# Kernel optimization log

Measured on AMD Instinct MI355X. Metric: run time of the kernel, lower is better.

## Reference

```python
import jax, jax.numpy as jnp
import numpy as np

IN_CH, HID, OUT = 128, 128, 47

def _sage_conv(x_src, x_dst, src, dst, n_dst, Wl, bl, Wr):
    # mean aggregation of source features onto destination nodes
    msg_sum = jax.ops.segment_sum(x_src[src], dst, num_segments=n_dst)
    deg = jax.ops.segment_sum(jnp.ones((src.shape[0],), x_src.dtype), dst, num_segments=n_dst)
    agg = msg_sum / jnp.maximum(deg, 1.0)[:, None]
    return agg @ Wl + bl + x_dst @ Wr


def setup_inputs() -> dict:
    key = jax.random.key(0)
    ks = jax.random.split(key, 12)
    N0, N1, N2 = 200000, 100000, 20000
    E0, E1 = 1600000, 320000
    def glorot(k, fan_in, fan_out):
        s = jnp.sqrt(6.0 / (fan_in + fan_out))
        return jax.random.uniform(k, (fan_in, fan_out), jnp.float32, -s, s)
    return {
        'x': jax.random.normal(ks[0], (N0, IN_CH), jnp.float32),
        'src0': jax.random.randint(ks[1], (E0,), 0, N0),
        'dst0': jax.random.randint(ks[2], (E0,), 0, N1),
        'src1': jax.random.randint(ks[3], (E1,), 0, N1),
        'dst1': jax.random.randint(ks[4], (E1,), 0, N2),
        'n1': N1,
        'n2': N2,
        'Wl0': glorot(ks[5], IN_CH, HID),
        'bl0': jnp.zeros((HID,), jnp.float32),
        'Wr0': glorot(ks[6], IN_CH, HID),
        'Wl1': glorot(ks[7], HID, OUT),
        'bl1': jnp.zeros((OUT,), jnp.float32),
        'Wr1': glorot(ks[8], HID, OUT),
    }


def reference(x, src0, dst0, src1, dst1, n1, n2, Wl0, bl0, Wr0, Wl1, bl1, Wr1):
    # layer 0: bipartite SAGEConv + relu (dropout is identity in eval mode)
    h = _sage_conv(x, x[:n1], src0, dst0, n1, Wl0, bl0, Wr0)
    h = jax.nn.relu(h)
    # layer 1: SAGEConv to output classes
    out = _sage_conv(h, h[:n2], src1, dst1, n2, Wl1, bl1, Wr1)
    return jax.nn.log_softmax(out, axis=-1)
```

## Files before the change

kernel.cpp:

```cpp
#include <hip/hip_runtime.h>
#include <hip/hip_bf16.h>
#include <math.h>

#define N1_ROWS 100000
#define N2_ROWS 20000
#define CH 128
#define OUTC 47
#define BSH 7
#define BROWS 128
#define CAP 2560
#define NBMX 1024
#define SCHUNK 4096

typedef __attribute__((ext_vector_type(8))) short short8;
typedef __attribute__((ext_vector_type(4))) float floatx4;

__device__ inline ushort f2b(float f) {
    union { __hip_bfloat16 b; ushort u; } cv;
    cv.b = __float2bfloat16(f);
    return cv.u;
}
__device__ inline float b2f_lo(uint u) { return __uint_as_float(u << 16); }
__device__ inline float b2f_hi(uint u) { return __uint_as_float(u & 0xffff0000u); }

__device__ inline void scatter_body(
    const int* __restrict__ src, const int* __restrict__ dst,
    uint* __restrict__ gcur, uint* __restrict__ ebuf, int E, int NB,
    int sb, uint* hist, uint* runb)
{
    const int base = sb * SCHUNK;
    const int t = threadIdx.x;

    uint d[16], s[16];
    bool ok[4];
    #pragma unroll
    for (int j = 0; j < 4; ++j) {
        int e = base + j * 1024 + t * 4;
        ok[j] = (e < E);
        if (ok[j]) {
            uint4 dv = *(const uint4*)(dst + e);
            uint4 sv = *(const uint4*)(src + e);
            d[j*4+0] = dv.x; d[j*4+1] = dv.y; d[j*4+2] = dv.z; d[j*4+3] = dv.w;
            s[j*4+0] = sv.x; s[j*4+1] = sv.y; s[j*4+2] = sv.z; s[j*4+3] = sv.w;
        }
    }

    for (int b = t; b < NBMX; b += 256) hist[b] = 0;
    __syncthreads();
    #pragma unroll
    for (int j = 0; j < 4; ++j)
        if (ok[j]) {
            #pragma unroll
            for (int k = 0; k < 4; ++k) atomicAdd(&hist[d[j*4+k] >> BSH], 1u);
        }
    __syncthreads();
    for (int b = t; b < NB; b += 256) {
        uint c = hist[b];
        runb[b] = c ? atomicAdd(&gcur[b], c) : 0u;
        hist[b] = 0;
    }
    __syncthreads();
    #pragma unroll
    for (int j = 0; j < 4; ++j)
        if (ok[j]) {
            #pragma unroll
            for (int k = 0; k < 4; ++k) {
                uint dd = d[j*4+k];
                uint b = dd >> BSH;
                uint off = runb[b] + atomicAdd(&hist[b], 1u);
                if (off < CAP)
                    ebuf[(size_t)b * CAP + off] = ((dd & (BROWS - 1u)) << 18) | s[j*4+k];
            }
        }
}

__global__ __launch_bounds__(256) void prep(
    const float* __restrict__ x, ushort* __restrict__ xb, int n4,
    const int* __restrict__ src0, const int* __restrict__ dst0,
    uint* __restrict__ gcur0, uint* __restrict__ ebuf0, int E0, int NB0,
    const int* __restrict__ src1, const int* __restrict__ dst1,
    uint* __restrict__ gcur1, uint* __restrict__ ebuf1, int E1, int NB1,
    const float* __restrict__ Wl0, const float* __restrict__ Wr0,
    const float* __restrict__ Wl1, const float* __restrict__ Wr1,
    const float* __restrict__ bl1,
    ushort* __restrict__ W0p, ushort* __restrict__ W1p, float* __restrict__ bl1p,
    int CB, int S0, int S1)
{
    __shared__ uint hist[NBMX];
    __shared__ uint runb[NBMX];
    int blk = blockIdx.x;
    if (blk < S0) {
        scatter_body(src0, dst0, gcur0, ebuf0, E0, NB0, blk, hist, runb);
    } else if (blk < S0 + S1) {
        scatter_body(src1, dst1, gcur1, ebuf1, E1, NB1, blk - S0, hist, runb);
    } else if (blk == S0 + S1) {
        int t = threadIdx.x;
        for (int c = t; c < 4096; c += 256) {
            int n = c & 127; int kb = (c >> 7) & 15; int p = c >> 11;
            const float* W = p ? Wr0 : Wl0;
            __align__(16) ushort tmp[8];
            #pragma unroll
            for (int i = 0; i < 8; ++i) tmp[i] = f2b(W[(kb * 8 + i) * CH + n]);
            *(uint4*)(W0p + (size_t)c * 8) = *(const uint4*)tmp;
        }
    } else if (blk == S0 + S1 + 1) {
        int t = threadIdx.x;
        for (int c = t; c < 1536; c += 256) {
            int n = c % 48; int kb = (c / 48) & 15; int p = c / 768;
            const float* W = p ? Wr1 : Wl1;
            __align__(16) ushort tmp[8];
            #pragma unroll
            for (int i = 0; i < 8; ++i)
                tmp[i] = (n < OUTC) ? f2b(W[(kb * 8 + i) * OUTC + n]) : (ushort)0;
            *(uint4*)(W1p + (size_t)c * 8) = *(const uint4*)tmp;
        }
        if (t < 48) bl1p[t] = (t < OUTC) ? bl1[t] : -3.0e38f;
    } else {
        int i = (blk - S0 - S1 - 2) * 256 + threadIdx.x;
        if (i < n4) {
            float4 v = ((const float4*)x)[i];
            ushort4 o;
            o.x = f2b(v.x); o.y = f2b(v.y); o.z = f2b(v.z); o.w = f2b(v.w);
            ((ushort4*)xb)[i] = o;
        }
    }
}

__global__ __launch_bounds__(512) void csr_gather(
    const uint* __restrict__ ebuf0, const uint* __restrict__ gcur0,
    const ushort* __restrict__ xb, ushort* __restrict__ aggb, int NB0, int n1,
    const uint* __restrict__ ebuf1, const uint* __restrict__ gcur1,
    int* __restrict__ idx1, int* __restrict__ deg1, int* __restrict__ rs1,
    int NB1, int n2)
{
    int t = threadIdx.x;
    __shared__ uint idxl[CAP];
    __shared__ uint hist[BROWS];
    __shared__ uint sc[BROWS];
    __shared__ uint lrs[BROWS];
    __shared__ uint degl[BROWS];
    __shared__ uint psc[256];

    int b = blockIdx.x;
    if (b < NB0) {
        uint cnt = gcur0[b]; if (cnt > CAP) cnt = CAP;
        size_t bin = (size_t)b * CAP;

        if (t < BROWS) hist[t] = 0;
        __syncthreads();
        for (uint i0 = 0; i0 < cnt; i0 += 2048) {
            uint i = i0 + t * 4;
            uint v0 = 0, v1 = 0, v2 = 0, v3 = 0; int nv = 0;
            if (i + 3 < cnt) {
                uint4 vv = *(const uint4*)(ebuf0 + bin + i);
                v0 = vv.x; v1 = vv.y; v2 = vv.z; v3 = vv.w; nv = 4;
            } else if (i < cnt) {
                nv = (int)(cnt - i);
                v0 = ebuf0[bin + i];
                if (nv > 1) v1 = ebuf0[bin + i + 1];
                if (nv > 2) v2 = ebuf0[bin + i + 2];
            }
            if (nv > 0) atomicAdd(&hist[v0 >> 18], 1u);
            if (nv > 1) atomicAdd(&hist[v1 >> 18], 1u);
            if (nv > 2) atomicAdd(&hist[v2 >> 18], 1u);
            if (nv > 3) atomicAdd(&hist[v3 >> 18], 1u);
        }
        __syncthreads();
        uint hv = 0;
        if (t < BROWS) { hv = hist[t]; sc[t] = hv; }
        __syncthreads();
        for (int off = 1; off < BROWS; off <<= 1) {
            uint val = 0;
            if (t < BROWS && t >= off) val = sc[t - off];
            __syncthreads();
            if (t < BROWS) sc[t] += val;
            __syncthreads();
        }
        if (t < BROWS) { lrs[t] = sc[t] - hv; degl[t] = hv; hist[t] = 0; }
        __syncthreads();
        for (uint i0 = 0; i0 < cnt; i0 += 2048) {
            uint i = i0 + t * 4;
            uint v0 = 0, v1 = 0, v2 = 0, v3 = 0; int nv = 0;
            if (i + 3 < cnt) {
                uint4 vv = *(const uint4*)(ebuf0 + bin + i);
                v0 = vv.x; v1 = vv.y; v2 = vv.z; v3 = vv.w; nv = 4;
            } else if (i < cnt) {
                nv = (int)(cnt - i);
                v0 = ebuf0[bin + i];
                if (nv > 1) v1 = ebuf0[bin + i + 1];
                if (nv > 2) v2 = ebuf0[bin + i + 2];
            }
            if (nv > 0) { uint r = v0 >> 18; idxl[lrs[r] + atomicAdd(&hist[r], 1u)] = v0 & 0x3FFFFu; }
            if (nv > 1) { uint r = v1 >> 18; idxl[lrs[r] + atomicAdd(&hist[r], 1u)] = v1 & 0x3FFFFu; }
            if (nv > 2) { uint r = v2 >> 18; idxl[lrs[r] + atomicAdd(&hist[r], 1u)] = v2 & 0x3FFFFu; }
            if (nv > 3) { uint r = v3 >> 18; idxl[lrs[r] + atomicAdd(&hist[r], 1u)] = v3 & 0x3FFFFu; }
        }
        __syncthreads();

        int wave = t >> 6, lane = t & 63;
        const int g  = lane >> 4;
        const int sl = lane & 15;
        const int gid = wave * 4 + g;
        const uint4* x4 = (const uint4*)xb;
        #pragma unroll 1
        for (int k = 0; k < 4; ++k) {
            int r = gid + 32 * k;
            int row = (b << BSH) + r;
            if (row >= n1) break;
            int start = (int)lrs[r];
            int cnt_r = (int)degl[r];
            float a0 = 0.f, a1 = 0.f, a2 = 0.f, a3 = 0.f;
            float a4 = 0.f, a5 = 0.f, a6 = 0.f, a7 = 0.f;
            int i = 0;
            for (; i + 3 < cnt_r; i += 4) {
                uint s0 = idxl[start + i];
                uint s1 = idxl[start + i + 1];
                uint s2 = idxl[start + i + 2];
                uint s3 = idxl[start + i + 3];
                uint4 v0 = x4[(size_t)s0 * 16 + sl];
                uint4 v1 = x4[(size_t)s1 * 16 + sl];
                uint4 v2 = x4[(size_t)s2 * 16 + sl];
                uint4 v3 = x4[(size_t)s3 * 16 + sl];
                a0 += (b2f_lo(v0.x) + b2f_lo(v1.x)) + (b2f_lo(v2.x) + b2f_lo(v3.x));
                a1 += (b2f_hi(v0.x) + b2f_hi(v1.x)) + (b2f_hi(v2.x) + b2f_hi(v3.x));
                a2 += (b2f_lo(v0.y) + b2f_lo(v1.y)) + (b2f_lo(v2.y) + b2f_lo(v3.y));
                a3 += (b2f_hi(v0.y) + b2f_hi(v1.y)) + (b2f_hi(v2.y) + b2f_hi(v3.y));
                a4 += (b2f_lo(v0.z) + b2f_lo(v1.z)) + (b2f_lo(v2.z) + b2f_lo(v3.z));
                a5 += (b2f_hi(v0.z) + b2f_hi(v1.z)) + (b2f_hi(v2.z) + b2f_hi(v3.z));
                a6 += (b2f_lo(v0.w) + b2f_lo(v1.w)) + (b2f_lo(v2.w) + b2f_lo(v3.w));
                a7 += (b2f_hi(v0.w) + b2f_hi(v1.w)) + (b2f_hi(v2.w) + b2f_hi(v3.w));
            }
            for (; i < cnt_r; ++i) {
                uint s0 = idxl[start + i];
                uint4 v0 = x4[(size_t)s0 * 16 + sl];
                a0 += b2f_lo(v0.x); a1 += b2f_hi(v0.x);
                a2 += b2f_lo(v0.y); a3 += b2f_hi(v0.y);
                a4 += b2f_lo(v0.z); a5 += b2f_hi(v0.z);
                a6 += b2f_lo(v0.w); a7 += b2f_hi(v0.w);
            }
            float inv = 1.0f / fmaxf((float)cnt_r, 1.0f);
            uint4 o;
            o.x = (uint)f2b(a0 * inv) | ((uint)f2b(a1 * inv) << 16);
            o.y = (uint)f2b(a2 * inv) | ((uint)f2b(a3 * inv) << 16);
            o.z = (uint)f2b(a4 * inv) | ((uint)f2b(a5 * inv) << 16);
            o.w = (uint)f2b(a6 * inv) | ((uint)f2b(a7 * inv) << 16);
            ((uint4*)aggb)[(size_t)row * 16 + sl] = o;
        }
    } else {
        b -= NB0;
        if (t < 256) {
            uint c = (t < NB1) ? gcur1[t] : 0u; if (c > CAP) c = CAP;
            psc[t] = c;
        }
        __syncthreads();
        for (int off = 1; off < 256; off <<= 1) {
            uint val = 0;
            if (t < 256 && t >= off) val = psc[t - off];
            __syncthreads();
            if (t < 256) psc[t] += val;
            __syncthreads();
        }
        uint cnt = gcur1[b]; if (cnt > CAP) cnt = CAP;
        uint bout = psc[b] - cnt;
        size_t bin = (size_t)b * CAP;
        int row0 = b << BSH;
        int nrows = n2 - row0; if (nrows > BROWS) nrows = BROWS;

        if (t < BROWS) hist[t] = 0;
        __syncthreads();
        for (uint i0 = 0; i0 < cnt; i0 += 2048) {
            uint i = i0 + t * 4;
            uint v0 = 0, v1 = 0, v2 = 0, v3 = 0; int nv = 0;
            if (i + 3 < cnt) {
                uint4 vv = *(const uint4*)(ebuf1 + bin + i);
                v0 = vv.x; v1 = vv.y; v2 = vv.z; v3 = vv.w; nv = 4;
            } else if (i < cnt) {
                nv = (int)(cnt - i);
                v0 = ebuf1[bin + i];
                if (nv > 1) v1 = ebuf1[bin + i + 1];
                if (nv > 2) v2 = ebuf1[bin + i + 2];
            }
            if (nv > 0) atomicAdd(&hist[v0 >> 18], 1u);
            if (nv > 1) atomicAdd(&hist[v1 >> 18], 1u);
            if (nv > 2) atomicAdd(&hist[v2 >> 18], 1u);
            if (nv > 3) atomicAdd(&hist[v3 >> 18], 1u);
        }
        __syncthreads();
        uint hv = 0;
        if (t < BROWS) { hv = hist[t]; sc[t] = hv; }
        __syncthreads();
        for (int off = 1; off < BROWS; off <<= 1) {
            uint val = 0;
            if (t < BROWS && t >= off) val = sc[t - off];
            __syncthreads();
            if (t < BROWS) sc[t] += val;
            __syncthreads();
        }
        if (t < BROWS) {
            uint lb = sc[t] - hv;
            lrs[t] = lb;
            if (t < nrows) { deg1[row0 + t] = (int)hv; rs1[row0 + t] = (int)(bout + lb); }
            hist[t] = 0;
        }
        __syncthreads();
        for (uint i0 = 0; i0 < cnt; i0 += 2048) {
            uint i = i0 + t * 4;
            uint v0 = 0, v1 = 0, v2 = 0, v3 = 0; int nv = 0;
            if (i + 3 < cnt) {
                uint4 vv = *(const uint4*)(ebuf1 + bin + i);
                v0 = vv.x; v1 = vv.y; v2 = vv.z; v3 = vv.w; nv = 4;
            } else if (i < cnt) {
                nv = (int)(cnt - i);
                v0 = ebuf1[bin + i];
                if (nv > 1) v1 = ebuf1[bin + i + 1];
                if (nv > 2) v2 = ebuf1[bin + i + 2];
            }
            if (nv > 0) { uint r = v0 >> 18; idxl[lrs[r] + atomicAdd(&hist[r], 1u)] = v0 & 0x3FFFFu; }
            if (nv > 1) { uint r = v1 >> 18; idxl[lrs[r] + atomicAdd(&hist[r], 1u)] = v1 & 0x3FFFFu; }
            if (nv > 2) { uint r = v2 >> 18; idxl[lrs[r] + atomicAdd(&hist[r], 1u)] = v2 & 0x3FFFFu; }
            if (nv > 3) { uint r = v3 >> 18; idxl[lrs[r] + atomicAdd(&hist[r], 1u)] = v3 & 0x3FFFFu; }
        }
        __syncthreads();
        for (uint i = t; i < cnt; i += 512) idx1[bout + i] = (int)idxl[i];
    }
}

__global__ __launch_bounds__(256) void gather_mean_bb(
    const ushort* __restrict__ xb,
    const int* __restrict__ idx,
    const int* __restrict__ rs,
    const int* __restrict__ deg,
    ushort* __restrict__ aggb,
    int n)
{
    int lane = threadIdx.x & 63;
    int wave = threadIdx.x >> 6;
    const int g  = lane >> 4;
    const int sl = lane & 15;
    int row = blockIdx.x * 16 + wave * 4 + g;
    if (row >= n) return;
    int start = rs[row];
    int cnt = deg[row];
    const uint4* x4 = (const uint4*)xb;
    float a0 = 0.f, a1 = 0.f, a2 = 0.f, a3 = 0.f;
    float a4 = 0.f, a5 = 0.f, a6 = 0.f, a7 = 0.f;
    int i = 0;
    for (; i + 3 < cnt; i += 4) {
        int s0 = idx[start + i];
        int s1 = idx[start + i + 1];
        int s2 = idx[start + i + 2];
        int s3 = idx[start + i + 3];
        uint4 v0 = x4[(size_t)s0 * 16 + sl];
        uint4 v1 = x4[(size_t)s1 * 16 + sl];
        uint4 v2 = x4[(size_t)s2 * 16 + sl];
        uint4 v3 = x4[(size_t)s3 * 16 + sl];
        a0 += (b2f_lo(v0.x) + b2f_lo(v1.x)) + (b2f_lo(v2.x) + b2f_lo(v3.x));
        a1 += (b2f_hi(v0.x) + b2f_hi(v1.x)) + (b2f_hi(v2.x) + b2f_hi(v3.x));
        a2 += (b2f_lo(v0.y) + b2f_lo(v1.y)) + (b2f_lo(v2.y) + b2f_lo(v3.y));
        a3 += (b2f_hi(v0.y) + b2f_hi(v1.y)) + (b2f_hi(v2.y) + b2f_hi(v3.y));
        a4 += (b2f_lo(v0.z) + b2f_lo(v1.z)) + (b2f_lo(v2.z) + b2f_lo(v3.z));
        a5 += (b2f_hi(v0.z) + b2f_hi(v1.z)) + (b2f_hi(v2.z) + b2f_hi(v3.z));
        a6 += (b2f_lo(v0.w) + b2f_lo(v1.w)) + (b2f_lo(v2.w) + b2f_lo(v3.w));
        a7 += (b2f_hi(v0.w) + b2f_hi(v1.w)) + (b2f_hi(v2.w) + b2f_hi(v3.w));
    }
    for (; i < cnt; ++i) {
        int s0 = idx[start + i];
        uint4 v0 = x4[(size_t)s0 * 16 + sl];
        a0 += b2f_lo(v0.x); a1 += b2f_hi(v0.x);
        a2 += b2f_lo(v0.y); a3 += b2f_hi(v0.y);
        a4 += b2f_lo(v0.z); a5 += b2f_hi(v0.z);
        a6 += b2f_lo(v0.w); a7 += b2f_hi(v0.w);
    }
    float inv = 1.0f / fmaxf((float)cnt, 1.0f);
    uint4 o;
    o.x = (uint)f2b(a0 * inv) | ((uint)f2b(a1 * inv) << 16);
    o.y = (uint)f2b(a2 * inv) | ((uint)f2b(a3 * inv) << 16);
    o.z = (uint)f2b(a4 * inv) | ((uint)f2b(a5 * inv) << 16);
    o.w = (uint)f2b(a6 * inv) | ((uint)f2b(a7 * inv) << 16);
    ((uint4*)aggb)[(size_t)row * 16 + sl] = o;
}

#define TM 128
__global__ __launch_bounds__(256) void gemm_mfma(
    const ushort* __restrict__ Apan,
    const ushort* __restrict__ Bpan,
    const ushort* __restrict__ Wp,
    const float* __restrict__ bias,
    ushort* __restrict__ H,
    int rows)
{
    __shared__ __align__(16) ushort As[16384];
    __shared__ __align__(16) ushort Ws[16384];

    const int tid = threadIdx.x;
    const int lane = tid & 63;
    const int wave = tid >> 6;
    const int q = lane >> 4;
    const int ln = lane & 15;
    const int rbase = blockIdx.x * TM;
    const int mrow = wave * 32;

    floatx4 acc[2][8];
    #pragma unroll
    for (int i = 0; i < 2; ++i)
        #pragma unroll
        for (int j = 0; j < 8; ++j)
            acc[i][j] = (floatx4)0.0f;

    #pragma unroll 1
    for (int phase = 0; phase < 2; ++phase) {
        const ushort* Ag = phase ? Bpan : Apan;

        {
            int m0 = tid & 15;
            int c  = tid >> 4;
            #pragma unroll
            for (int j = 0; j < 8; ++j) {
                int m = m0 + 16 * j;
                uint4 v = *(const uint4*)(Ag + (size_t)(rbase + m) * CH + c * 8);
                *(uint4*)(As + ((size_t)c * 128 + m) * 8) = v;
            }
        }
        {
            const uint4* Wg4 = (const uint4*)(Wp + phase * 16384);
            uint4* Ws4 = (uint4*)Ws;
            for (int i = tid; i < 2048; i += 256) Ws4[i] = Wg4[i];
        }
        __syncthreads();

        #pragma unroll
        for (int k = 0; k < 4; ++k) {
            int kb = k * 4 + q;
            short8 b[8];
            #pragma unroll
            for (int nt = 0; nt < 8; ++nt)
                b[nt] = *(const short8*)(Ws + ((size_t)kb * 128 + nt * 16 + ln) * 8);
            #pragma unroll
            for (int mt = 0; mt < 2; ++mt) {
                short8 a = *(const short8*)(As + ((size_t)kb * 128 + mrow + mt * 16 + ln) * 8);
                #pragma unroll
                for (int nt = 0; nt < 8; ++nt)
                    acc[mt][nt] = __builtin_amdgcn_mfma_f32_16x16x32_bf16(
                        a, b[nt], acc[mt][nt], 0, 0, 0);
            }
        }
        __syncthreads();
    }

    float bj[8];
    #pragma unroll
    for (int nt = 0; nt < 8; ++nt) bj[nt] = bias[nt * 16 + ln];

    #pragma unroll
    for (int mt = 0; mt < 2; ++mt) {
        #pragma unroll
        for (int r = 0; r < 4; ++r) {
            int grow = rbase + mrow + mt * 16 + q * 4 + r;
            if (grow < rows) {
                #pragma unroll
                for (int nt = 0; nt < 8; ++nt) {
                    float v = acc[mt][nt][r] + bj[nt];
                    v = fmaxf(v, 0.0f);
                    H[(size_t)grow * CH + nt * 16 + ln] = f2b(v);
                }
            }
        }
    }
}

__global__ __launch_bounds__(256) void gemm_mfma_l1(
    const ushort* __restrict__ Apan,
    const ushort* __restrict__ Bpan,
    const ushort* __restrict__ Wp,
    const float* __restrict__ biasp,
    float* __restrict__ out,
    int rows)
{
    __shared__ __align__(16) ushort As[16384];
    __shared__ __align__(16) ushort Ws[6144];

    const int tid = threadIdx.x;
    const int lane = tid & 63;
    const int wave = tid >> 6;
    const int q = lane >> 4;
    const int ln = lane & 15;
    const int rbase = blockIdx.x * TM;
    const int mrow = wave * 32;

    floatx4 acc[2][3];
    #pragma unroll
    for (int i = 0; i < 2; ++i)
        #pragma unroll
        for (int j = 0; j < 3; ++j)
            acc[i][j] = (floatx4)0.0f;

    #pragma unroll 1
    for (int phase = 0; phase < 2; ++phase) {
        const ushort* Ag = phase ? Bpan : Apan;
        {
            int m0 = tid & 15;
            int c  = tid >> 4;
            #pragma unroll
            for (int j = 0; j < 8; ++j) {
                int m = m0 + 16 * j;
                uint4 v = *(const uint4*)(Ag + (size_t)(rbase + m) * CH + c * 8);
                *(uint4*)(As + ((size_t)c * 128 + m) * 8) = v;
            }
        }
        {
            const uint4* Wg4 = (const uint4*)(Wp + phase * 6144);
            uint4* Ws4 = (uint4*)Ws;
            for (int i = tid; i < 768; i += 256) Ws4[i] = Wg4[i];
        }
        __syncthreads();

        #pragma unroll
        for (int k = 0; k < 4; ++k) {
            int kb = k * 4 + q;
            short8 b0 = *(const short8*)(Ws + ((size_t)kb * 48 +  0 + ln) * 8);
            short8 b1 = *(const short8*)(Ws + ((size_t)kb * 48 + 16 + ln) * 8);
            short8 b2 = *(const short8*)(Ws + ((size_t)kb * 48 + 32 + ln) * 8);
            #pragma unroll
            for (int mt = 0; mt < 2; ++mt) {
                short8 a = *(const short8*)(As + ((size_t)kb * 128 + mrow + mt * 16 + ln) * 8);
                acc[mt][0] = __builtin_amdgcn_mfma_f32_16x16x32_bf16(a, b0, acc[mt][0], 0, 0, 0);
                acc[mt][1] = __builtin_amdgcn_mfma_f32_16x16x32_bf16(a, b1, acc[mt][1], 0, 0, 0);
                acc[mt][2] = __builtin_amdgcn_mfma_f32_16x16x32_bf16(a, b2, acc[mt][2], 0, 0, 0);
            }
        }
        __syncthreads();
    }

    float b0 = biasp[ln], b1 = biasp[16 + ln], b2 = biasp[32 + ln];

    #pragma unroll
    for (int mt = 0; mt < 2; ++mt) {
        #pragma unroll
        for (int r = 0; r < 4; ++r) {
            int grow = rbase + mrow + mt * 16 + q * 4 + r;
            float v0 = acc[mt][0][r] + b0;
            float v1 = acc[mt][1][r] + b1;
            float v2 = acc[mt][2][r] + b2;
            float mx = fmaxf(v0, fmaxf(v1, v2));
            #pragma unroll
            for (int off = 1; off < 16; off <<= 1) mx = fmaxf(mx, __shfl_xor(mx, off));
            float s = expf(v0 - mx) + expf(v1 - mx) + expf(v2 - mx);
            #pragma unroll
            for (int off = 1; off < 16; off <<= 1) s += __shfl_xor(s, off);
            float ls = mx + logf(s);
            if (grow < rows) {
                out[(size_t)grow * OUTC + ln] = v0 - ls;
                out[(size_t)grow * OUTC + 16 + ln] = v1 - ls;
                if (32 + ln < OUTC) out[(size_t)grow * OUTC + 32 + ln] = v2 - ls;
            }
        }
    }
}

extern "C" void kernel_launch(void* const* d_in, const int* in_sizes, int n_in,
                              void* d_out, int out_size, void* d_ws, size_t ws_size,
                              hipStream_t stream) {
    const float* x    = (const float*)d_in[0];
    const int*   src0 = (const int*)d_in[1];
    const int*   dst0 = (const int*)d_in[2];
    const int*   src1 = (const int*)d_in[3];
    const int*   dst1 = (const int*)d_in[4];
    const float* Wl0  = (const float*)d_in[7];
    const float* bl0  = (const float*)d_in[8];
    const float* Wr0  = (const float*)d_in[9];
    const float* Wl1  = (const float*)d_in[10];
    const float* bl1  = (const float*)d_in[11];
    const float* Wr1  = (const float*)d_in[12];
    float* out = (float*)d_out;

    const int E0 = in_sizes[1];
    const int E1 = in_sizes[3];
    const int n0 = in_sizes[0] / CH;
    const int n1 = N1_ROWS, n2 = N2_ROWS;
    const int n1pad = ((n1 + TM - 1) / TM) * TM;
    const int n2pad = ((n2 + TM - 1) / TM) * TM;
    const int NB0 = (n1 + BROWS - 1) >> BSH;
    const int NB1 = (n2 + BROWS - 1) >> BSH;

    ushort* xb   = (ushort*)d_ws;
    ushort* aggb = xb + (size_t)n0 * CH;
    ushort* h    = aggb + (size_t)n1pad * CH;
    ushort* W0p  = h + (size_t)n1 * CH;
    ushort* W1p  = W0p + 32768;
    float*  bl1p = (float*)(W1p + 12288);
    int*    idx1 = (int*)(bl1p + 48);
    int*    deg1 = idx1 + E1;
    int*    rs1  = deg1 + n2;
    uint*   gcur0 = (uint*)(rs1 + n2);
    uint*   gcur1 = gcur0 + NBMX;

    uint* ebuf0 = (uint*)h;
    uint* ebuf1 = (uint*)h + (size_t)NB0 * CAP;
    ushort* agg1b = aggb;

    const int n4 = n0 * CH / 4;
    const int CB = (n4 + 255) / 256;
    const int S0 = (E0 + SCHUNK - 1) / SCHUNK;
    const int S1 = (E1 + SCHUNK - 1) / SCHUNK;

    hipMemsetAsync(gcur0, 0, 2 * NBMX * sizeof(uint), stream);
    prep<<<S0 + S1 + 2 + CB, 256, 0, stream>>>(
        x, xb, n4,
        src0, dst0, gcur0, ebuf0, E0, NB0,
        src1, dst1, gcur1, ebuf1, E1, NB1,
        Wl0, Wr0, Wl1, Wr1, bl1, W0p, W1p, bl1p,
        CB, S0, S1);
    csr_gather<<<NB0 + NB1, 512, 0, stream>>>(
        ebuf0, gcur0, xb, aggb, NB0, n1,
        ebuf1, gcur1, idx1, deg1, rs1, NB1, n2);
    gemm_mfma<<<n1pad / TM, 256, 0, stream>>>(aggb, xb, W0p, bl0, h, n1);
    gather_mean_bb<<<(n2 + 15) / 16, 256, 0, stream>>>(h, idx1, rs1, deg1, agg1b, n2);
    gemm_mfma_l1<<<n2pad / TM, 256, 0, stream>>>(agg1b, h, W1p, bl1p, out, n2);
}
```

Measured before the change: 316.2 us.

## Fuse layer-0 CSR gather with MFMA GEMM into a single kernel

The layer-0 mean aggregation now writes its bf16 result straight into shared memory in the MFMA panel layout, and the same block then runs the two-phase GEMM (aggregated features times Wl, then x rows times Wr) with bias and ReLU. This removes the separate gemm_mfma launch and the global round trip through the aggregation buffer. Edge buffers get their own workspace region because h is now written while ebuf is still in use. The cost is much more shared memory per 512-thread block (about 64 KB extra), which may lower occupancy of the latency-bound gather phase.

```diff
diff --git a/kernel.cpp b/kernel.cpp
--- a/kernel.cpp
+++ b/kernel.cpp
@@ -126,9 +126,12 @@
     }
 }
 
-__global__ __launch_bounds__(512) void csr_gather(
-    const uint* __restrict__ ebuf0, const uint* __restrict__ gcur0,
-    const ushort* __restrict__ xb, ushort* __restrict__ aggb, int NB0, int n1,
+__global__ __launch_bounds__(512) void fused0(
+    const uint* __restrict__ ebuf, const uint* __restrict__ gcur,
+    const ushort* __restrict__ xb,
+    const ushort* __restrict__ Wp,
+    const float* __restrict__ bias,
+    ushort* __restrict__ H, int n1, int NB0,
     const uint* __restrict__ ebuf1, const uint* __restrict__ gcur1,
     int* __restrict__ idx1, int* __restrict__ deg1, int* __restrict__ rs1,
     int NB1, int n2)
@@ -140,11 +143,19 @@
     __shared__ uint lrs[BROWS];
     __shared__ uint degl[BROWS];
     __shared__ uint psc[256];
+    __shared__ __align__(16) ushort As[16384];
+    __shared__ __align__(16) ushort Ws[16384];
 
     int b = blockIdx.x;
     if (b < NB0) {
-        uint cnt = gcur0[b]; if (cnt > CAP) cnt = CAP;
+        uint cnt = gcur[b]; if (cnt > CAP) cnt = CAP;
         size_t bin = (size_t)b * CAP;
+
+        {
+            const uint4* Wg4 = (const uint4*)Wp;
+            uint4* Ws4 = (uint4*)Ws;
+            for (int i = t; i < 2048; i += 512) Ws4[i] = Wg4[i];
+        }
 
         if (t < BROWS) hist[t] = 0;
         __syncthreads();
@@ -152,13 +163,13 @@
             uint i = i0 + t * 4;
             uint v0 = 0, v1 = 0, v2 = 0, v3 = 0; int nv = 0;
             if (i + 3 < cnt) {
-                uint4 vv = *(const uint4*)(ebuf0 + bin + i);
+                uint4 vv = *(const uint4*)(ebuf + bin + i);
                 v0 = vv.x; v1 = vv.y; v2 = vv.z; v3 = vv.w; nv = 4;
             } else if (i < cnt) {
                 nv = (int)(cnt - i);
-                v0 = ebuf0[bin + i];
-                if (nv > 1) v1 = ebuf0[bin + i + 1];
-                if (nv > 2) v2 = ebuf0[bin + i + 2];
+                v0 = ebuf[bin + i];
+                if (nv > 1) v1 = ebuf[bin + i + 1];
+                if (nv > 2) v2 = ebuf[bin + i + 2];
             }
             if (nv > 0) atomicAdd(&hist[v0 >> 18], 1u);
             if (nv > 1) atomicAdd(&hist[v1 >> 18], 1u);
@@ -182,13 +193,13 @@
             uint i = i0 + t * 4;
             uint v0 = 0, v1 = 0, v2 = 0, v3 = 0; int nv = 0;
             if (i + 3 < cnt) {
-                uint4 vv = *(const uint4*)(ebuf0 + bin + i);
+                uint4 vv = *(const uint4*)(ebuf + bin + i);
                 v0 = vv.x; v1 = vv.y; v2 = vv.z; v3 = vv.w; nv = 4;
             } else if (i < cnt) {
                 nv = (int)(cnt - i);
-                v0 = ebuf0[bin + i];
-                if (nv > 1) v1 = ebuf0[bin + i + 1];
-                if (nv > 2) v2 = ebuf0[bin + i + 2];
+                v0 = ebuf[bin + i];
+                if (nv > 1) v1 = ebuf[bin + i + 1];
+                if (nv > 2) v2 = ebuf[bin + i + 2];
             }
             if (nv > 0) { uint r = v0 >> 18; idxl[lrs[r] + atomicAdd(&hist[r], 1u)] = v0 & 0x3FFFFu; }
             if (nv > 1) { uint r = v1 >> 18; idxl[lrs[r] + atomicAdd(&hist[r], 1u)] = v1 & 0x3FFFFu; }
@@ -206,45 +217,103 @@
         for (int k = 0; k < 4; ++k) {
             int r = gid + 32 * k;
             int row = (b << BSH) + r;
-            if (row >= n1) break;
-            int start = (int)lrs[r];
-            int cnt_r = (int)degl[r];
-            float a0 = 0.f, a1 = 0.f, a2 = 0.f, a3 = 0.f;
-            float a4 = 0.f, a5 = 0.f, a6 = 0.f, a7 = 0.f;
-            int i = 0;
-            for (; i + 3 < cnt_r; i += 4) {
-                uint s0 = idxl[start + i];
-                uint s1 = idxl[start + i + 1];
-                uint s2 = idxl[start + i + 2];
-                uint s3 = idxl[start + i + 3];
-                uint4 v0 = x4[(size_t)s0 * 16 + sl];
-                uint4 v1 = x4[(size_t)s1 * 16 + sl];
-                uint4 v2 = x4[(size_t)s2 * 16 + sl];
-                uint4 v3 = x4[(size_t)s3 * 16 + sl];
-                a0 += (b2f_lo(v0.x) + b2f_lo(v1.x)) + (b2f_lo(v2.x) + b2f_lo(v3.x));
-                a1 += (b2f_hi(v0.x) + b2f_hi(v1.x)) + (b2f_hi(v2.x) + b2f_hi(v3.x));
-                a2 += (b2f_lo(v0.y) + b2f_lo(v1.y)) + (b2f_lo(v2.y) + b2f_lo(v3.y));
-                a3 += (b2f_hi(v0.y) + b2f_hi(v1.y)) + (b2f_hi(v2.y) + b2f_hi(v3.y));
-                a4 += (b2f_lo(v0.z) + b2f_lo(v1.z)) + (b2f_lo(v2.z) + b2f_lo(v3.z));
-                a5 += (b2f_hi(v0.z) + b2f_hi(v1.z)) + (b2f_hi(v2.z) + b2f_hi(v3.z));
-                a6 += (b2f_lo(v0.w) + b2f_lo(v1.w)) + (b2f_lo(v2.w) + b2f_lo(v3.w));
-                a7 += (b2f_hi(v0.w) + b2f_hi(v1.w)) + (b2f_hi(v2.w) + b2f_hi(v3.w));
-            }
-            for (; i < cnt_r; ++i) {
-                uint s0 = idxl[start + i];
-                uint4 v0 = x4[(size_t)s0 * 16 + sl];
-                a0 += b2f_lo(v0.x); a1 += b2f_hi(v0.x);
-                a2 += b2f_lo(v0.y); a3 += b2f_hi(v0.y);
-                a4 += b2f_lo(v0.z); a5 += b2f_hi(v0.z);
-                a6 += b2f_lo(v0.w); a7 += b2f_hi(v0.w);
-            }
-            float inv = 1.0f / fmaxf((float)cnt_r, 1.0f);
-            uint4 o;
-            o.x = (uint)f2b(a0 * inv) | ((uint)f2b(a1 * inv) << 16);
-            o.y = (uint)f2b(a2 * inv) | ((uint)f2b(a3 * inv) << 16);
-            o.z = (uint)f2b(a4 * inv) | ((uint)f2b(a5 * inv) << 16);
-            o.w = (uint)f2b(a6 * inv) | ((uint)f2b(a7 * inv) << 16);
-            ((uint4*)aggb)[(size_t)row * 16 + sl] = o;
+            if (row < n1) {
+                int start = (int)lrs[r];
+                int cnt_r = (int)degl[r];
+                float a0 = 0.f, a1 = 0.f, a2 = 0.f, a3 = 0.f;
+                float a4 = 0.f, a5 = 0.f, a6 = 0.f, a7 = 0.f;
+                int i = 0;
+                for (; i + 3 < cnt_r; i += 4) {
+                    uint s0 = idxl[start + i];
+                    uint s1 = idxl[start + i + 1];
+                    uint s2 = idxl[start + i + 2];
+                    uint s3 = idxl[start + i + 3];
+                    uint4 v0 = x4[(size_t)s0 * 16 + sl];
+                    uint4 v1 = x4[(size_t)s1 * 16 + sl];
+                    uint4 v2 = x4[(size_t)s2 * 16 + sl];
+                    uint4 v3 = x4[(size_t)s3 * 16 + sl];
+                    a0 += (b2f_lo(v0.x) + b2f_lo(v1.x)) + (b2f_lo(v2.x) + b2f_lo(v3.x));
+                    a1 += (b2f_hi(v0.x) + b2f_hi(v1.x)) + (b2f_hi(v2.x) + b2f_hi(v3.x));
+                    a2 += (b2f_lo(v0.y) + b2f_lo(v1.y)) + (b2f_lo(v2.y) + b2f_lo(v3.y));
+                    a3 += (b2f_hi(v0.y) + b2f_hi(v1.y)) + (b2f_hi(v2.y) + b2f_hi(v3.y));
+                    a4 += (b2f_lo(v0.z) + b2f_lo(v1.z)) + (b2f_lo(v2.z) + b2f_lo(v3.z));
+                    a5 += (b2f_hi(v0.z) + b2f_hi(v1.z)) + (b2f_hi(v2.z) + b2f_hi(v3.z));
+                    a6 += (b2f_lo(v0.w) + b2f_lo(v1.w)) + (b2f_lo(v2.w) + b2f_lo(v3.w));
+                    a7 += (b2f_hi(v0.w) + b2f_hi(v1.w)) + (b2f_hi(v2.w) + b2f_hi(v3.w));
+                }
+                for (; i < cnt_r; ++i) {
+                    uint s0 = idxl[start + i];
+                    uint4 v0 = x4[(size_t)s0 * 16 + sl];
+                    a0 += b2f_lo(v0.x); a1 += b2f_hi(v0.x);
+                    a2 += b2f_lo(v0.y); a3 += b2f_hi(v0.y);
+                    a4 += b2f_lo(v0.z); a5 += b2f_hi(v0.z);
+                    a6 += b2f_lo(v0.w); a7 += b2f_hi(v0.w);
+                }
+                float inv = 1.0f / fmaxf((float)cnt_r, 1.0f);
+                uint4 o;
+                o.x = (uint)f2b(a0 * inv) | ((uint)f2b(a1 * inv) << 16);
+                o.y = (uint)f2b(a2 * inv) | ((uint)f2b(a3 * inv) << 16);
+                o.z = (uint)f2b(a4 * inv) | ((uint)f2b(a5 * inv) << 16);
+                o.w = (uint)f2b(a6 * inv) | ((uint)f2b(a7 * inv) << 16);
+                *(uint4*)(As + ((size_t)sl * 128 + r) * 8) = o;
+            }
+        }
+
+        const int q = g, ln = sl;
+        const int rbase = b << BSH;
+        const int mrow = wave * 16;
+        floatx4 acc[8];
+        #pragma unroll
+        for (int nt = 0; nt < 8; ++nt) acc[nt] = (floatx4)0.0f;
+
+        #pragma unroll 1
+        for (int phase = 0; phase < 2; ++phase) {
+            if (phase == 1) {
+                __syncthreads();
+                {
+                    int m0 = t & 15, c = (t >> 4) & 15, jb = (t >> 8) * 4;
+                    #pragma unroll
+                    for (int j = 0; j < 4; ++j) {
+                        int m = m0 + 16 * (jb + j);
+                        uint4 v = *(const uint4*)(xb + (size_t)(rbase + m) * CH + c * 8);
+                        *(uint4*)(As + ((size_t)c * 128 + m) * 8) = v;
+                    }
+                }
+                {
+                    const uint4* Wg4 = (const uint4*)(Wp + 16384);
+                    uint4* Ws4 = (uint4*)Ws;
+                    for (int i = t; i < 2048; i += 512) Ws4[i] = Wg4[i];
+                }
+            }
+            __syncthreads();
+            #pragma unroll
+            for (int k = 0; k < 4; ++k) {
+                int kb = k * 4 + q;
+                short8 bb[8];
+                #pragma unroll
+                for (int nt = 0; nt < 8; ++nt)
+                    bb[nt] = *(const short8*)(Ws + ((size_t)kb * 128 + nt * 16 + ln) * 8);
+                short8 a = *(const short8*)(As + ((size_t)kb * 128 + mrow + ln) * 8);
+                #pragma unroll
+                for (int nt = 0; nt < 8; ++nt)
+                    acc[nt] = __builtin_amdgcn_mfma_f32_16x16x32_bf16(a, bb[nt], acc[nt], 0, 0, 0);
+            }
+        }
+
+        float bj[8];
+        #pragma unroll
+        for (int nt = 0; nt < 8; ++nt) bj[nt] = bias[nt * 16 + ln];
+        #pragma unroll
+        for (int r = 0; r < 4; ++r) {
+            int grow = rbase + mrow + q * 4 + r;
+            if (grow < n1) {
+                #pragma unroll
+                for (int nt = 0; nt < 8; ++nt) {
+                    float v = acc[nt][r] + bj[nt];
+                    v = fmaxf(v, 0.0f);
+                    H[(size_t)grow * CH + nt * 16 + ln] = f2b(v);
+                }
+            }
         }
     } else {
         b -= NB0;
@@ -381,93 +450,6 @@
 }
 
 #define TM 128
-__global__ __launch_bounds__(256) void gemm_mfma(
-    const ushort* __restrict__ Apan,
-    const ushort* __restrict__ Bpan,
-    const ushort* __restrict__ Wp,
-    const float* __restrict__ bias,
-    ushort* __restrict__ H,
-    int rows)
-{
-    __shared__ __align__(16) ushort As[16384];
-    __shared__ __align__(16) ushort Ws[16384];
-
-    const int tid = threadIdx.x;
-    const int lane = tid & 63;
-    const int wave = tid >> 6;
-    const int q = lane >> 4;
-    const int ln = lane & 15;
-    const int rbase = blockIdx.x * TM;
-    const int mrow = wave * 32;
-
-    floatx4 acc[2][8];
-    #pragma unroll
-    for (int i = 0; i < 2; ++i)
-        #pragma unroll
-        for (int j = 0; j < 8; ++j)
-            acc[i][j] = (floatx4)0.0f;
-
-    #pragma unroll 1
-    for (int phase = 0; phase < 2; ++phase) {
-        const ushort* Ag = phase ? Bpan : Apan;
-
-        {
-            int m0 = tid & 15;
-            int c  = tid >> 4;
-            #pragma unroll
-            for (int j = 0; j < 8; ++j) {
-                int m = m0 + 16 * j;
-                uint4 v = *(const uint4*)(Ag + (size_t)(rbase + m) * CH + c * 8);
-                *(uint4*)(As + ((size_t)c * 128 + m) * 8) = v;
-            }
-        }
-        {
-            const uint4* Wg4 = (const uint4*)(Wp + phase * 16384);
-            uint4* Ws4 = (uint4*)Ws;
-            for (int i = tid; i < 2048; i += 256) Ws4[i] = Wg4[i];
-        }
-        __syncthreads();
-
-        #pragma unroll
-        for (int k = 0; k < 4; ++k) {
-            int kb = k * 4 + q;
-            short8 b[8];
-            #pragma unroll
-            for (int nt = 0; nt < 8; ++nt)
-                b[nt] = *(const short8*)(Ws + ((size_t)kb * 128 + nt * 16 + ln) * 8);
-            #pragma unroll
-            for (int mt = 0; mt < 2; ++mt) {
-                short8 a = *(const short8*)(As + ((size_t)kb * 128 + mrow + mt * 16 + ln) * 8);
-                #pragma unroll
-                for (int nt = 0; nt < 8; ++nt)
-                    acc[mt][nt] = __builtin_amdgcn_mfma_f32_16x16x32_bf16(
-                        a, b[nt], acc[mt][nt], 0, 0, 0);
-            }
-        }
-        __syncthreads();
-    }
-
-    float bj[8];
-    #pragma unroll
-    for (int nt = 0; nt < 8; ++nt) bj[nt] = bias[nt * 16 + ln];
-
-    #pragma unroll
-    for (int mt = 0; mt < 2; ++mt) {
-        #pragma unroll
-        for (int r = 0; r < 4; ++r) {
-            int grow = rbase + mrow + mt * 16 + q * 4 + r;
-            if (grow < rows) {
-                #pragma unroll
-                for (int nt = 0; nt < 8; ++nt) {
-                    float v = acc[mt][nt][r] + bj[nt];
-                    v = fmaxf(v, 0.0f);
-                    H[(size_t)grow * CH + nt * 16 + ln] = f2b(v);
-                }
-            }
-        }
-    }
-}
-
 __global__ __launch_bounds__(256) void gemm_mfma_l1(
     const ushort* __restrict__ Apan,
     const ushort* __restrict__ Bpan,
@@ -577,14 +559,12 @@
     const int E1 = in_sizes[3];
     const int n0 = in_sizes[0] / CH;
     const int n1 = N1_ROWS, n2 = N2_ROWS;
-    const int n1pad = ((n1 + TM - 1) / TM) * TM;
     const int n2pad = ((n2 + TM - 1) / TM) * TM;
     const int NB0 = (n1 + BROWS - 1) >> BSH;
     const int NB1 = (n2 + BROWS - 1) >> BSH;
 
     ushort* xb   = (ushort*)d_ws;
-    ushort* aggb = xb + (size_t)n0 * CH;
-    ushort* h    = aggb + (size_t)n1pad * CH;
+    ushort* h    = xb + (size_t)n0 * CH;
     ushort* W0p  = h + (size_t)n1 * CH;
     ushort* W1p  = W0p + 32768;
     float*  bl1p = (float*)(W1p + 12288);
@@ -593,10 +573,9 @@
     int*    rs1  = deg1 + n2;
     uint*   gcur0 = (uint*)(rs1 + n2);
     uint*   gcur1 = gcur0 + NBMX;
-
-    uint* ebuf0 = (uint*)h;
-    uint* ebuf1 = (uint*)h + (size_t)NB0 * CAP;
-    ushort* agg1b = aggb;
+    uint*   ebuf0 = gcur1 + NBMX;
+    uint*   ebuf1 = ebuf0 + (size_t)NB0 * CAP;
+    ushort* agg1b = (ushort*)(ebuf1 + (size_t)NB1 * CAP);
 
     const int n4 = n0 * CH / 4;
     const int CB = (n4 + 255) / 256;
@@ -610,10 +589,9 @@
         src1, dst1, gcur1, ebuf1, E1, NB1,
         Wl0, Wr0, Wl1, Wr1, bl1, W0p, W1p, bl1p,
         CB, S0, S1);
-    csr_gather<<<NB0 + NB1, 512, 0, stream>>>(
-        ebuf0, gcur0, xb, aggb, NB0, n1,
+    fused0<<<NB0 + NB1, 512, 0, stream>>>(
+        ebuf0, gcur0, xb, W0p, bl0, h, n1, NB0,
         ebuf1, gcur1, idx1, deg1, rs1, NB1, n2);
-    gemm_mfma<<<n1pad / TM, 256, 0, stream>>>(aggb, xb, W0p, bl0, h, n1);
     gather_mean_bb<<<(n2 + 15) / 16, 256, 0, stream>>>(h, idx1, rs1, deg1, agg1b, n2);
     gemm_mfma_l1<<<n2pad / TM, 256, 0, stream>>>(agg1b, h, W1p, bl1p, out, n2);
 }
```

Result: faster. 301.1 us (-4.8%).
